# Performance work log

Measured on AMD Instinct MI355X. Metric: run time of the kernel, lower is better.

## Reference

```python
import jax, jax.numpy as jnp
import numpy as np
from jax import lax

BETA = 0.95     # snn.Leaky(0.95)
THRESH = 1.0    # snntorch default threshold
ALPHA = 2.0     # snntorch ATan surrogate default alpha
NUM_STEPS = 100

@jax.custom_vjp
def spike_fn(u):
    return (u > 0).astype(u.dtype)

def _spike_fwd(u):
    return (u > 0).astype(u.dtype), u

def _spike_bwd(u, g):
    surr = (ALPHA / 2.0) / (1.0 + (jnp.pi / 2.0 * ALPHA * u) ** 2)
    return (g * surr,)

spike_fn.defvjp(_spike_fwd, _spike_bwd)

def leaky_scan(inputs, mem0):
    # inputs: [T, ...]; snntorch Leaky with reset_mechanism='zero'
    def step(carry, x_t):
        mem, _ = carry
        reset = spike_fn(mem - THRESH)       # spike detected from previous mem
        base = BETA * mem + x_t
        mem = base - reset * base            # zero-reset
        spk = spike_fn(mem - THRESH)
        return (mem, spk), None
    (mem, spk), _ = lax.scan(step, (mem0, jnp.zeros_like(mem0)), inputs)
    return spk, mem

def setup_inputs():
    key = jax.random.key(0)
    ks = jax.random.split(key, 7)
    B, T, W, C = 32, 2000, 512, 4
    H, O = 1024, 10
    s = lambda n: 1.0 / np.sqrt(n)
    return {
        "x": jax.random.normal(ks[0], (B, T, W, C), jnp.float32),
        "conv_w": jax.random.uniform(ks[1], (C,), jnp.float32, -s(C), s(C)),
        "conv_b": jax.random.uniform(ks[2], (), jnp.float32, -s(C), s(C)),
        "hidden_w": jax.random.uniform(ks[3], (H, W), jnp.float32, -s(W), s(W)),
        "hidden_b": jax.random.uniform(ks[4], (H,), jnp.float32, -s(W), s(W)),
        "out_w": jax.random.uniform(ks[5], (O, H), jnp.float32, -s(H), s(H)),
        "out_b": jax.random.uniform(ks[6], (O,), jnp.float32, -s(H), s(H)),
    }

def reference(x, conv_w, conv_b, hidden_w, hidden_b, out_w, out_b):
    B, T, W, _ = x.shape
    # 1x1 conv fusing 4 antenna channels: (B,T,W,4)->(B,T,W)
    fused = jnp.einsum('bhwc,c->bhw', x, conv_w) + conv_b
    G = T // NUM_STEPS
    fused = fused.reshape(B, G, NUM_STEPS, W)      # [B,G,S,W]
    seq1 = jnp.moveaxis(fused, 2, 0)               # [S,B,G,W] time-major
    spk, _ = leaky_scan(seq1, jnp.zeros((B, G, W), x.dtype))
    hidden = spk @ hidden_w.T + hidden_b           # [B,G,H]
    seq2 = jnp.moveaxis(hidden, 1, 0)              # [G,B,H]
    spk2, _ = leaky_scan(seq2, jnp.zeros((B, hidden.shape[2]), x.dtype))
    out = spk2 @ out_w.T + out_b                   # [B,O]
    return jax.nn.softmax(out, axis=1)
```

## Files before the change

kernel.cpp:

```cpp
#include <hip/hip_runtime.h>
#include <hip/hip_bf16.h>

typedef float f32x4 __attribute__((ext_vector_type(4)));

#define NB 32
#define NT 2000
#define NW 512
#define NG 20
#define NS 100
#define NH 1024
#define NO 10
#define BETA 0.95f
#define THRESH 1.0f

__global__ __launch_bounds__(256) void k1_conv_scan_tr(
    const f32x4* __restrict__ x,
    const float* __restrict__ cw,
    const float* __restrict__ cb,
    float* __restrict__ spk1,
    const float* __restrict__ wsrc,
    float* __restrict__ wT)
{
    __shared__ float tile[32][33];
    int bid = blockIdx.x;

    if (bid < 1280) {
        int half = bid & 1;
        int bg = bid >> 1;
        int g = bg % NG;
        int b = bg / NG;
        int tid = threadIdx.x;

        const f32x4* __restrict__ base =
            x + ((size_t)(b * NT + g * NS) * NW + half * 256);

        float w0 = cw[0], w1 = cw[1], w2 = cw[2], w3 = cw[3];
        float bias = cb[0];

        f32x4 A[10], B[10];
        float mem = 0.0f;

#define LOAD10(dst, S0)                                                        \
    {                                                                          \
        _Pragma("unroll")                                                      \
        for (int j = 0; j < 10; ++j)                                           \
            dst[j] = __builtin_nontemporal_load(base + (tid + ((S0) + j) * NW)); \
    }
#define STEP10(src)                                                            \
    {                                                                          \
        _Pragma("unroll")                                                      \
        for (int j = 0; j < 10; ++j) {                                         \
            f32x4 v = src[j];                                                  \
            float f = fmaf(v[0], w0, fmaf(v[1], w1,                            \
                      fmaf(v[2], w2, fmaf(v[3], w3, bias))));                  \
            float base_m = fmaf(BETA, mem, f);                                 \
            mem = (mem > THRESH) ? 0.0f : base_m;                              \
        }                                                                      \
    }

        LOAD10(A, 0)
        LOAD10(B, 10) STEP10(A)
        LOAD10(A, 20) STEP10(B)
        LOAD10(B, 30) STEP10(A)
        LOAD10(A, 40) STEP10(B)
        LOAD10(B, 50) STEP10(A)
        LOAD10(A, 60) STEP10(B)
        LOAD10(B, 70) STEP10(A)
        LOAD10(A, 80) STEP10(B)
        LOAD10(B, 90) STEP10(A)
        STEP10(B)
#undef LOAD10
#undef STEP10

        spk1[(b * NG + g) * NW + half * 256 + tid] = (mem > THRESH) ? 1.0f : 0.0f;
    } else {
        int tbid = bid - 1280;
        int bk = tbid & 15;
        int bh = tbid >> 4;
        int tx = threadIdx.x & 31;
        int ty = threadIdx.x >> 5;
        #pragma unroll
        for (int j = 0; j < 4; ++j)
            tile[ty + j * 8][tx] = wsrc[(bh * 32 + ty + j * 8) * NW + bk * 32 + tx];
        __syncthreads();
        #pragma unroll
        for (int j = 0; j < 4; ++j)
            wT[(bk * 32 + ty + j * 8) * NH + bh * 32 + tx] = tile[tx][ty + j * 8];
    }
}

__global__ __launch_bounds__(256) void k2_hidden_scan(
    const float* __restrict__ spk1,
    const float* __restrict__ wT,
    const float* __restrict__ hb,
    const float* __restrict__ ow,
    float* __restrict__ partial)
{
    __shared__ float sk[NG][NW];
    __shared__ float red[4][NG][64];

    int bid = blockIdx.x;
    int b = bid >> 4;
    int hgrp = bid & 15;
    int t = threadIdx.x;
    int lane5 = t & 31;
    int c = t >> 5;
    int h = hgrp * 64 + lane5 * 2;

    {
        const f32x4* __restrict__ sp4 =
            (const f32x4*)(spk1 + (size_t)b * NG * NW);
        f32x4* sk4 = (f32x4*)&sk[0][0];
        #pragma unroll
        for (int i = 0; i < 10; ++i)
            sk4[t + i * 256] = sp4[t + i * 256];
    }
    __syncthreads();

    float2 acc[NG];
    #pragma unroll
    for (int g = 0; g < NG; ++g) { acc[g].x = 0.0f; acc[g].y = 0.0f; }

    int k0 = c * 64;
    #pragma unroll 2
    for (int kkg = 0; kkg < 16; ++kkg) {
        int kk = k0 + kkg * 4;
        float2 a0 = *(const float2*)&wT[(kk + 0) * NH + h];
        float2 a1 = *(const float2*)&wT[(kk + 1) * NH + h];
        float2 a2 = *(const float2*)&wT[(kk + 2) * NH + h];
        float2 a3 = *(const float2*)&wT[(kk + 3) * NH + h];
        #pragma unroll
        for (int g = 0; g < NG; ++g) {
            f32x4 u = *(const f32x4*)&sk[g][kk];
            acc[g].x = fmaf(u[0], a0.x, fmaf(u[1], a1.x,
                       fmaf(u[2], a2.x, fmaf(u[3], a3.x, acc[g].x))));
            acc[g].y = fmaf(u[0], a0.y, fmaf(u[1], a1.y,
                       fmaf(u[2], a2.y, fmaf(u[3], a3.y, acc[g].y))));
        }
    }

    if (c < 4) {
        #pragma unroll
        for (int g = 0; g < NG; ++g)
            *(float2*)&red[c][g][lane5 * 2] = acc[g];
    }
    __syncthreads();
    if (c >= 4) {
        #pragma unroll
        for (int g = 0; g < NG; ++g) {
            float2 v = *(float2*)&red[c - 4][g][lane5 * 2];
            v.x += acc[g].x; v.y += acc[g].y;
            *(float2*)&red[c - 4][g][lane5 * 2] = v;
        }
    }
    __syncthreads();

    if (t < 64) {
        float hbias = hb[hgrp * 64 + t];
        float mem = 0.0f;
        #pragma unroll
        for (int g = 0; g < NG; ++g) {
            float xin = red[0][g][t] + red[1][g][t]
                      + red[2][g][t] + red[3][g][t] + hbias;
            float base = fmaf(BETA, mem, xin);
            mem = (mem > THRESH) ? 0.0f : base;
        }
        float spike = (mem > THRESH) ? 1.0f : 0.0f;

        #pragma unroll
        for (int o = 0; o < NO; ++o) {
            float p = spike * ow[o * NH + hgrp * 64 + t];
            p += __shfl_down(p, 32);
            p += __shfl_down(p, 16);
            p += __shfl_down(p, 8);
            p += __shfl_down(p, 4);
            p += __shfl_down(p, 2);
            p += __shfl_down(p, 1);
            if (t == 0) partial[(b * 16 + hgrp) * NO + o] = p;
        }
    }
}

__global__ __launch_bounds__(64) void k_softmax(
    const float* __restrict__ partial,
    const float* __restrict__ ob,
    float* __restrict__ out)
{
    int t = threadIdx.x;
    if (t < NB) {
        const float* p = partial + t * 16 * NO;
        float v[NO];
        #pragma unroll
        for (int o = 0; o < NO; ++o) v[o] = ob[o];
        #pragma unroll
        for (int hg = 0; hg < 16; ++hg)
            #pragma unroll
            for (int o = 0; o < NO; ++o) v[o] += p[hg * NO + o];

        float mx = -1e30f;
        #pragma unroll
        for (int o = 0; o < NO; ++o) mx = fmaxf(mx, v[o]);
        float sum = 0.0f;
        #pragma unroll
        for (int o = 0; o < NO; ++o) { v[o] = expf(v[o] - mx); sum += v[o]; }
        float inv = 1.0f / sum;
        #pragma unroll
        for (int o = 0; o < NO; ++o) out[t * NO + o] = v[o] * inv;
    }
}

extern "C" void kernel_launch(void* const* d_in, const int* in_sizes, int n_in,
                              void* d_out, int out_size, void* d_ws, size_t ws_size,
                              hipStream_t stream) {
    const f32x4*  x  = (const f32x4*)d_in[0];
    const float*  cw = (const float*)d_in[1];
    const float*  cb = (const float*)d_in[2];
    const float*  hw = (const float*)d_in[3];
    const float*  hb = (const float*)d_in[4];
    const float*  ow = (const float*)d_in[5];
    const float*  ob = (const float*)d_in[6];
    float* out = (float*)d_out;

    char* ws = (char*)d_ws;
    float* spk1    = (float*)(ws);
    float* wT      = (float*)(ws + 1310720);
    float* partial = (float*)(ws + 1310720 + 2097152);

    k1_conv_scan_tr<<<1792, 256, 0, stream>>>(x, cw, cb, spk1, hw, wT);

    k2_hidden_scan<<<NB * 16, 256, 0, stream>>>(spk1, wT, hb, ow, partial);

    k_softmax<<<1, 64, 0, stream>>>(partial, ob, out);
}
```

Measured before the change: 103.6 us.

## Fuse softmax into hidden kernel via last-block atomic, widen hidden GEMV tiling

Removes the separate softmax launch: each hidden-layer block bumps a global counter, and the last block to finish computes the softmax. The counter is reset inside the first kernel. The hidden GEMV now gives each thread 4 output columns over 16 K-chunks of 32 instead of 2 columns over 8 chunks of 64. It also rotates the K order per thread group to spread shared-memory bank accesses, and reuses the skip buffer's shared memory for the reduction. This saves a kernel launch and improves weight-load vectorization, at the cost of more accumulator registers and an atomic plus fence per block.

```diff
diff --git a/kernel.cpp b/kernel.cpp
--- a/kernel.cpp
+++ b/kernel.cpp
@@ -19,7 +19,8 @@
     const float* __restrict__ cb,
     float* __restrict__ spk1,
     const float* __restrict__ wsrc,
-    float* __restrict__ wT)
+    float* __restrict__ wT,
+    int* __restrict__ counter)
 {
     __shared__ float tile[32][33];
     int bid = blockIdx.x;
@@ -75,6 +76,7 @@
         spk1[(b * NG + g) * NW + half * 256 + tid] = (mem > THRESH) ? 1.0f : 0.0f;
     } else {
         int tbid = bid - 1280;
+        if (tbid == 0 && threadIdx.x == 0) *counter = 0;
         int bk = tbid & 15;
         int bh = tbid >> 4;
         int tx = threadIdx.x & 31;
@@ -94,74 +96,84 @@
     const float* __restrict__ wT,
     const float* __restrict__ hb,
     const float* __restrict__ ow,
-    float* __restrict__ partial)
+    const float* __restrict__ ob,
+    float* __restrict__ partial,
+    int* __restrict__ counter,
+    float* __restrict__ out)
 {
-    __shared__ float sk[NG][NW];
-    __shared__ float red[4][NG][64];
+    __shared__ __align__(16) char smem[40960];
+    float (*sk)[NW]     = (float (*)[NW])smem;
+    f32x4 (*red)[NG][16] = (f32x4 (*)[NG][16])smem;
+    __shared__ int lastFlag;
 
     int bid = blockIdx.x;
     int b = bid >> 4;
     int hgrp = bid & 15;
     int t = threadIdx.x;
-    int lane5 = t & 31;
-    int c = t >> 5;
-    int h = hgrp * 64 + lane5 * 2;
+    int lane4 = t & 15;
+    int c = t >> 4;
+    int h = hgrp * 64 + lane4 * 4;
 
     {
         const f32x4* __restrict__ sp4 =
             (const f32x4*)(spk1 + (size_t)b * NG * NW);
-        f32x4* sk4 = (f32x4*)&sk[0][0];
+        f32x4* sk4 = (f32x4*)smem;
         #pragma unroll
         for (int i = 0; i < 10; ++i)
             sk4[t + i * 256] = sp4[t + i * 256];
     }
     __syncthreads();
 
-    float2 acc[NG];
+    f32x4 acc[NG];
     #pragma unroll
-    for (int g = 0; g < NG; ++g) { acc[g].x = 0.0f; acc[g].y = 0.0f; }
-
-    int k0 = c * 64;
-    #pragma unroll 2
-    for (int kkg = 0; kkg < 16; ++kkg) {
-        int kk = k0 + kkg * 4;
-        float2 a0 = *(const float2*)&wT[(kk + 0) * NH + h];
-        float2 a1 = *(const float2*)&wT[(kk + 1) * NH + h];
-        float2 a2 = *(const float2*)&wT[(kk + 2) * NH + h];
-        float2 a3 = *(const float2*)&wT[(kk + 3) * NH + h];
+    for (int g = 0; g < NG; ++g)
+        #pragma unroll
+        for (int j = 0; j < 4; ++j) acc[g][j] = 0.0f;
+
+    int k0 = c * 32;
+    #pragma unroll
+    for (int kkg = 0; kkg < 8; ++kkg) {
+        int kk = k0 + (((kkg + c) & 7) << 2);
+        f32x4 w0 = *(const f32x4*)&wT[(kk + 0) * NH + h];
+        f32x4 w1 = *(const f32x4*)&wT[(kk + 1) * NH + h];
+        f32x4 w2 = *(const f32x4*)&wT[(kk + 2) * NH + h];
+        f32x4 w3 = *(const f32x4*)&wT[(kk + 3) * NH + h];
         #pragma unroll
         for (int g = 0; g < NG; ++g) {
             f32x4 u = *(const f32x4*)&sk[g][kk];
-            acc[g].x = fmaf(u[0], a0.x, fmaf(u[1], a1.x,
-                       fmaf(u[2], a2.x, fmaf(u[3], a3.x, acc[g].x))));
-            acc[g].y = fmaf(u[0], a0.y, fmaf(u[1], a1.y,
-                       fmaf(u[2], a2.y, fmaf(u[3], a3.y, acc[g].y))));
-        }
-    }
-
-    if (c < 4) {
-        #pragma unroll
-        for (int g = 0; g < NG; ++g)
-            *(float2*)&red[c][g][lane5 * 2] = acc[g];
-    }
-    __syncthreads();
-    if (c >= 4) {
+            #pragma unroll
+            for (int j = 0; j < 4; ++j)
+                acc[g][j] = fmaf(u[0], w0[j], fmaf(u[1], w1[j],
+                            fmaf(u[2], w2[j], fmaf(u[3], w3[j], acc[g][j]))));
+        }
+    }
+
+    __syncthreads();
+    if (c < 8) {
+        #pragma unroll
+        for (int g = 0; g < NG; ++g) red[c][g][lane4] = acc[g];
+    }
+    __syncthreads();
+    if (c >= 8) {
         #pragma unroll
         for (int g = 0; g < NG; ++g) {
-            float2 v = *(float2*)&red[c - 4][g][lane5 * 2];
-            v.x += acc[g].x; v.y += acc[g].y;
-            *(float2*)&red[c - 4][g][lane5 * 2] = v;
+            f32x4 v = red[c - 8][g][lane4];
+            #pragma unroll
+            for (int j = 0; j < 4; ++j) v[j] += acc[g][j];
+            red[c - 8][g][lane4] = v;
         }
     }
     __syncthreads();
 
     if (t < 64) {
         float hbias = hb[hgrp * 64 + t];
+        int hl = t >> 2, hj = t & 3;
         float mem = 0.0f;
         #pragma unroll
         for (int g = 0; g < NG; ++g) {
-            float xin = red[0][g][t] + red[1][g][t]
-                      + red[2][g][t] + red[3][g][t] + hbias;
+            float xin = hbias;
+            #pragma unroll
+            for (int cc = 0; cc < 8; ++cc) xin += red[cc][g][hl][hj];
             float base = fmaf(BETA, mem, xin);
             mem = (mem > THRESH) ? 0.0f : base;
         }
@@ -179,33 +191,35 @@
             if (t == 0) partial[(b * 16 + hgrp) * NO + o] = p;
         }
     }
-}
-
-__global__ __launch_bounds__(64) void k_softmax(
-    const float* __restrict__ partial,
-    const float* __restrict__ ob,
-    float* __restrict__ out)
-{
-    int t = threadIdx.x;
-    if (t < NB) {
-        const float* p = partial + t * 16 * NO;
-        float v[NO];
-        #pragma unroll
-        for (int o = 0; o < NO; ++o) v[o] = ob[o];
-        #pragma unroll
-        for (int hg = 0; hg < 16; ++hg)
-            #pragma unroll
-            for (int o = 0; o < NO; ++o) v[o] += p[hg * NO + o];
-
-        float mx = -1e30f;
-        #pragma unroll
-        for (int o = 0; o < NO; ++o) mx = fmaxf(mx, v[o]);
-        float sum = 0.0f;
-        #pragma unroll
-        for (int o = 0; o < NO; ++o) { v[o] = expf(v[o] - mx); sum += v[o]; }
-        float inv = 1.0f / sum;
-        #pragma unroll
-        for (int o = 0; o < NO; ++o) out[t * NO + o] = v[o] * inv;
+
+    if (t == 0) {
+        __threadfence();
+        int old = atomicAdd(counter, 1);
+        lastFlag = (old == NB * 16 - 1);
+    }
+    __syncthreads();
+    if (lastFlag) {
+        __threadfence();
+        if (t < NB) {
+            const float* p = partial + t * 16 * NO;
+            float v[NO];
+            #pragma unroll
+            for (int o = 0; o < NO; ++o) v[o] = ob[o];
+            #pragma unroll
+            for (int hg = 0; hg < 16; ++hg)
+                #pragma unroll
+                for (int o = 0; o < NO; ++o) v[o] += p[hg * NO + o];
+
+            float mx = -1e30f;
+            #pragma unroll
+            for (int o = 0; o < NO; ++o) mx = fmaxf(mx, v[o]);
+            float sum = 0.0f;
+            #pragma unroll
+            for (int o = 0; o < NO; ++o) { v[o] = expf(v[o] - mx); sum += v[o]; }
+            float inv = 1.0f / sum;
+            #pragma unroll
+            for (int o = 0; o < NO; ++o) out[t * NO + o] = v[o] * inv;
+        }
     }
 }
 
@@ -225,10 +239,10 @@
     float* spk1    = (float*)(ws);
     float* wT      = (float*)(ws + 1310720);
     float* partial = (float*)(ws + 1310720 + 2097152);
-
-    k1_conv_scan_tr<<<1792, 256, 0, stream>>>(x, cw, cb, spk1, hw, wT);
-
-    k2_hidden_scan<<<NB * 16, 256, 0, stream>>>(spk1, wT, hb, ow, partial);
-
-    k_softmax<<<1, 64, 0, stream>>>(partial, ob, out);
+    int*   counter = (int*)(ws + 1310720 + 2097152 + 20480);
+
+    k1_conv_scan_tr<<<1792, 256, 0, stream>>>(x, cw, cb, spk1, hw, wT, counter);
+
+    k2_hidden_scan<<<NB * 16, 256, 0, stream>>>(spk1, wT, hb, ow, ob,
+                                                partial, counter, out);
 }
```

After: 110.4 us. +6.6%, slower.
